# Performance work log

Hardware: AMD Instinct MI355X
Metric: run time of the kernel (lower is better)

## Reference

```python
import jax, jax.numpy as jnp
import numpy as np
import math

B, L, DIM = 2, 2048, 1024
HEADS = 16
DH = DIM // HEADS  # 64
M_IALSH = 2
U_IALSH = 0.75
NEG = -1e4  # additive mask value for non-matching hash buckets


def setup_inputs() -> dict:
    key = jax.random.key(0)
    k0, k1, k2, k3 = jax.random.split(key, 4)
    return {
        "hidden_states": jax.random.normal(k0, (B, L, DIM), jnp.float32),
        "qk_w": jax.random.normal(k1, (DIM, DIM), jnp.float32) * 0.02,
        "qk_b": jnp.zeros((DIM,), jnp.float32),
        "v_w": jax.random.normal(k2, (DIM, DIM), jnp.float32) * 0.02,
        "v_b": jnp.zeros((DIM,), jnp.float32),
        "hash_a": jax.random.normal(k3, (DH + M_IALSH,), jnp.float32),
    }


def _ialsh_mask(qkh, hash_a):
    # qkh: (b, h, l, dh). IALSH (Improved Asymmetric LSH for MIPS):
    # keys scaled so max norm per (b,h) is U; P(x)=[x, 1/2-||x||^2, 1/2-||x||^4]
    # queries unit-normalized;        Q(x)=[x/||x||, 0, 0]
    norms = jnp.linalg.norm(qkh, axis=-1, keepdims=True)          # (b,h,l,1)
    max_norm = jnp.max(norms, axis=2, keepdims=True)              # (b,h,1,1)
    xk = qkh * (U_IALSH / jnp.maximum(max_norm, 1e-12))
    nk2 = jnp.sum(xk * xk, axis=-1, keepdims=True)                # ||x||^2
    P = jnp.concatenate([xk, 0.5 - nk2, 0.5 - nk2 * nk2], axis=-1)
    q_unit = qkh / jnp.maximum(norms, 1e-12)
    zeros = jnp.zeros_like(nk2)
    Q = jnp.concatenate([q_unit, zeros, zeros], axis=-1)
    hq = (Q @ hash_a) >= 0.0                                      # (b,h,l) sign hash
    hk = (P @ hash_a) >= 0.0
    same = hq[..., :, None] == hk[..., None, :]                   # (b,h,l,l)
    return jnp.where(same, 0.0, NEG).astype(qkh.dtype)


def reference(hidden_states, qk_w, qk_b, v_w, v_b, hash_a):
    b, l, d = hidden_states.shape
    qk = hidden_states @ qk_w.T + qk_b                            # shared Q/K projection
    v = hidden_states @ v_w.T + v_b

    def split(x):  # (b,l,d) -> (b,h,l,dh)
        return x.reshape(b, l, HEADS, DH).transpose(0, 2, 1, 3)

    qkh, vh = split(qk), split(v)
    scores = jnp.einsum('bhqd,bhkd->bhqk', qkh, qkh) / math.sqrt(DH)
    scores = scores + _ialsh_mask(qkh, hash_a)
    probs = jax.nn.softmax(scores, axis=-1)  # dropout = identity (eval mode)
    ctx = jnp.einsum('bhqk,bhkd->bhqd', probs, vh)
    return ctx.transpose(0, 2, 1, 3).reshape(b, l, d)
```

## Files before the change

kernel.cpp:

```cpp
#include <hip/hip_runtime.h>

typedef unsigned short u16;
typedef unsigned char  u8;
typedef unsigned int   u32;

typedef short bf16x8 __attribute__((ext_vector_type(8)));
typedef float f32x4  __attribute__((ext_vector_type(4)));

#define DEV __device__ __forceinline__

#if __has_builtin(__builtin_amdgcn_exp2f)
#define EXP2(x) __builtin_amdgcn_exp2f(x)
#else
#define EXP2(x) exp2f(x)
#endif

DEV u16 f2bf(float x) {
  u32 u = __builtin_bit_cast(u32, x);
  u32 r = (u + 0x7fffu + ((u >> 16) & 1u)) >> 16;
  return (u16)r;
}
DEV float bf2f(u16 h) {
  u32 u = ((u32)h) << 16;
  return __builtin_bit_cast(float, u);
}
DEV f32x4 mfma16(bf16x8 a, bf16x8 b, f32x4 c) {
  return __builtin_amdgcn_mfma_f32_16x16x32_bf16(a, b, c, 0, 0, 0);
}

#define GLDS(gptr, lptr)                                                  \
  __builtin_amdgcn_global_load_lds(                                       \
      (const __attribute__((address_space(1))) void*)(gptr),              \
      (__attribute__((address_space(3))) void*)(lptr), 16, 0, 0)

__global__ __launch_bounds__(256) void split3_kernel(
    const float* __restrict__ hid, const float* __restrict__ wq,
    const float* __restrict__ wv,
    u16* __restrict__ hHi, u16* __restrict__ hLo,
    u16* __restrict__ wqHi, u16* __restrict__ wqLo, u16* __restrict__ wvHi) {
  const int NH = 4194304, NW = 1048576;
  int i = blockIdx.x * 256 + threadIdx.x;
  if (i < NH) {
    float v = hid[i];
    u16 t = f2bf(v);
    hHi[i] = t;
    hLo[i] = f2bf(v - bf2f(t));
  } else if (i < NH + NW) {
    int j = i - NH;
    float v = wq[j];
    u16 t = f2bf(v);
    wqHi[j] = t;
    wqLo[j] = f2bf(v - bf2f(t));
  } else {
    int j = i - NH - NW;
    wvHi[j] = f2bf(wv[j]);
  }
}

__global__ __launch_bounds__(256) void ca_kernel(
    const float* __restrict__ W, const float* __restrict__ ha, double* __restrict__ ca) {
  int idx = blockIdx.x * 256 + threadIdx.x;
  int h = idx >> 10, k = idx & 1023;
  double s = 0.0;
#pragma unroll 8
  for (int j = 0; j < 64; ++j)
    s += (double)W[(size_t)(h * 64 + j) * 1024 + k] * (double)ha[j];
  ca[idx] = s;
}

__global__ __launch_bounds__(256) void d_kernel(
    const float* __restrict__ hid, const double* __restrict__ ca, float* __restrict__ dq) {
  const int row  = blockIdx.x * 4 + (threadIdx.x >> 6);
  const int lane = threadIdx.x & 63;
  const int b = row >> 11, l = row & 2047;
  double acc[16];
#pragma unroll
  for (int h = 0; h < 16; ++h) acc[h] = 0.0;
  const float* hp = hid + (size_t)row * 1024;
  for (int k = lane; k < 1024; k += 64) {
    const double hv = (double)hp[k];
#pragma unroll
    for (int h = 0; h < 16; ++h) acc[h] += hv * ca[h * 1024 + k];
  }
#pragma unroll
  for (int h = 0; h < 16; ++h) {
    double v = acc[h];
#pragma unroll
    for (int off = 32; off; off >>= 1) v += __shfl_xor(v, off, 64);
    if (lane == 0) dq[(size_t)(b * 16 + h) * 2048 + l] = (float)v;
  }
}

__global__ __launch_bounds__(256, 2) void gemm_fused(
    const u16* __restrict__ hHi, const u16* __restrict__ hLo,
    const u16* __restrict__ wqHi, const u16* __restrict__ wqLo,
    const u16* __restrict__ wvHi,
    const float* __restrict__ qk_b, const float* __restrict__ v_b,
    u16* __restrict__ qkB, u16* __restrict__ vT, float* __restrict__ n2A) {
  constexpr int K = 1024;
  __shared__ u16 S[2][16384];
  const int tid = threadIdx.x, wave = tid >> 6, lane = tid & 63;
  const int quad = lane >> 4, lm = lane & 15;
  const int wr = wave >> 1, wc = wave & 1;
  const int m0 = blockIdx.x * 64, n0 = blockIdx.y * 128;
  const int ch = lane & 3, rA = lane >> 2;

  auto stage = [&](int kt, int buf) {
    const int k0 = kt * 32;
    const int rowA = wave * 16 + rA;
    GLDS(hHi + (size_t)(m0 + rowA) * K + k0 + ch * 8, &S[buf][0 + wave * 512]);
    GLDS(hLo + (size_t)(m0 + rowA) * K + k0 + ch * 8, &S[buf][2048 + wave * 512]);
#pragma unroll
    for (int it = 0; it < 2; ++it) {
      const int rb = wave * 2 + it;
      const int row = rb * 16 + rA;
      GLDS(wqHi + (size_t)(n0 + row) * K + k0 + ch * 8, &S[buf][4096 + rb * 512]);
      GLDS(wqLo + (size_t)(n0 + row) * K + k0 + ch * 8, &S[buf][8192 + rb * 512]);
      GLDS(wvHi + (size_t)(n0 + row) * K + k0 + ch * 8, &S[buf][12288 + rb * 512]);
    }
  };

  f32x4 aq[2][4], av[4][2];
#pragma unroll
  for (int i = 0; i < 2; ++i)
#pragma unroll
    for (int j = 0; j < 4; ++j) aq[i][j] = {0.f, 0.f, 0.f, 0.f};
#pragma unroll
  for (int i = 0; i < 4; ++i)
#pragma unroll
    for (int j = 0; j < 2; ++j) av[i][j] = {0.f, 0.f, 0.f, 0.f};

  stage(0, 0);
  __syncthreads();

  for (int kt = 0; kt < 32; ++kt) {
    const int cur = kt & 1;
    if (kt < 31) stage(kt + 1, cur ^ 1);

    bf16x8 a_h[2], a_l[2], b_h[4], b_l[4], w_h[4];
#pragma unroll
    for (int i = 0; i < 2; ++i) {
      a_h[i] = *(const bf16x8*)&S[cur][(wr * 32 + i * 16 + lm) * 32 + quad * 8];
      a_l[i] = *(const bf16x8*)&S[cur][2048 + (wr * 32 + i * 16 + lm) * 32 + quad * 8];
    }
#pragma unroll
    for (int j = 0; j < 4; ++j) {
      b_h[j] = *(const bf16x8*)&S[cur][4096 + (wc * 64 + j * 16 + lm) * 32 + quad * 8];
      b_l[j] = *(const bf16x8*)&S[cur][8192 + (wc * 64 + j * 16 + lm) * 32 + quad * 8];
      w_h[j] = *(const bf16x8*)&S[cur][12288 + (wc * 64 + j * 16 + lm) * 32 + quad * 8];
    }
#pragma unroll
    for (int i = 0; i < 2; ++i)
#pragma unroll
      for (int j = 0; j < 4; ++j) {
        aq[i][j] = mfma16(a_h[i], b_h[j], aq[i][j]);
        aq[i][j] = mfma16(a_h[i], b_l[j], aq[i][j]);
        aq[i][j] = mfma16(a_l[i], b_h[j], aq[i][j]);
      }
#pragma unroll
    for (int iv = 0; iv < 4; ++iv)
#pragma unroll
      for (int jv = 0; jv < 2; ++jv)
        av[iv][jv] = mfma16(w_h[iv], a_h[jv], av[iv][jv]);

    __syncthreads();
  }

  const int hidx = blockIdx.y * 2 + wc;
#pragma unroll
  for (int i = 0; i < 2; ++i) {
    float nn[4] = {0.f, 0.f, 0.f, 0.f};
#pragma unroll
    for (int j = 0; j < 4; ++j) {
      const int col = n0 + wc * 64 + j * 16 + lm;
      const float bv = qk_b[col];
#pragma unroll
      for (int r = 0; r < 4; ++r) {
        const int row = m0 + wr * 32 + i * 16 + quad * 4 + r;
        const float val = aq[i][j][r] + bv;
        qkB[(size_t)row * 1024 + col] = f2bf(val);
        nn[r] += val * val;
      }
    }
#pragma unroll
    for (int r = 0; r < 4; ++r)
#pragma unroll
      for (int off = 1; off < 16; off <<= 1) nn[r] += __shfl_xor(nn[r], off, 64);
    if (lm == 0) {
      const int row = m0 + wr * 32 + i * 16 + quad * 4;
      const int b = row >> 11, l = row & 2047;
      *(float4*)&n2A[(size_t)(b * 16 + hidx) * 2048 + l] =
          make_float4(nn[0], nn[1], nn[2], nn[3]);
    }
  }
#pragma unroll
  for (int iv = 0; iv < 4; ++iv)
#pragma unroll
    for (int r = 0; r < 4; ++r) {
      const int vcol = n0 + wc * 64 + iv * 16 + quad * 4 + r;
      const float bv = v_b[vcol];
#pragma unroll
      for (int jv = 0; jv < 2; ++jv) {
        const int tok = m0 + wr * 32 + jv * 16 + lm;
        vT[(size_t)vcol * 4096 + tok] = f2bf(av[iv][jv][r] + bv);
      }
    }
}

__global__ __launch_bounds__(256) void bits_kernel(
    const float* __restrict__ n2A, const float* __restrict__ dq,
    const float* __restrict__ ha, u8* __restrict__ hqA, u8* __restrict__ hkA) {
  const int bh = blockIdx.x;
  const int tid = threadIdx.x;
  const int wave = tid >> 6, lane = tid & 63;
  __shared__ float red[4];
  const float* n2p = n2A + (size_t)bh * 2048;
  float4 v0 = ((const float4*)n2p)[tid];
  float4 v1 = ((const float4*)n2p)[tid + 256];
  float lmax = fmaxf(fmaxf(fmaxf(v0.x, v0.y), fmaxf(v0.z, v0.w)),
                     fmaxf(fmaxf(v1.x, v1.y), fmaxf(v1.z, v1.w)));
#pragma unroll
  for (int off = 1; off < 64; off <<= 1) lmax = fmaxf(lmax, __shfl_xor(lmax, off, 64));
  if (lane == 0) red[wave] = lmax;
  __syncthreads();
  const float maxn2 = fmaxf(fmaxf(red[0], red[1]), fmaxf(red[2], red[3]));
  const float s = 0.75f / fmaxf(sqrtf(maxn2), 1e-12f);
  const float a64 = ha[64], a65 = ha[65];
#pragma unroll
  for (int it = 0; it < 8; ++it) {
    const int l = it * 256 + tid;
    const float dv = dq[(size_t)bh * 2048 + l];
    const float n2 = n2p[l];
    const float nk2 = s * s * n2;
    const float hkdot = s * dv + (0.5f - nk2) * a64 + (0.5f - nk2 * nk2) * a65;
    hqA[(size_t)bh * 2048 + l] = (dv >= 0.f) ? 1 : 0;
    hkA[(size_t)bh * 2048 + l] = (hkdot >= 0.f) ? 1 : 0;
  }
}

__global__ __launch_bounds__(256, 4) void attn_kernel(
    const u16* __restrict__ qkb, const u16* __restrict__ vT,
    const u8* __restrict__ hqA, const u8* __restrict__ hkA, float* __restrict__ out) {
  __shared__ u16 Ks[2][4096];
  __shared__ u16 Vs[2][4096];
  __shared__ u16 Ps[4][1024];

  const int qt = blockIdx.x;
  const int bh = blockIdx.y;
  const int b = bh >> 4, h = bh & 15;
  const int tid = threadIdx.x, wave = tid >> 6, lane = tid & 63;
  const int quad = lane >> 4, lm = lane & 15;
  const int lx = lm & 7;
  const int r8 = lane >> 3, ch = lane & 7;
  const int q0 = qt * 64;

  const u16* qbase = qkb + (size_t)b * 2048 * 1024 + h * 64;
  const u16* vtb = vT + (size_t)h * 64 * 4096 + b * 2048;
  const u8* hkp = hkA + (size_t)bh * 2048;

  bf16x8 aQ[2];
#pragma unroll
  for (int c = 0; c < 2; ++c)
    aQ[c] = *(const bf16x8*)(qbase +
        (size_t)(q0 + wave * 16 + lm) * 1024 + c * 32 + quad * 8);
  u8 hqb[4];
  {
    const u8* hqp = hqA + (size_t)bh * 2048 + q0 + wave * 16;
#pragma unroll
    for (int r = 0; r < 4; ++r) hqb[r] = hqp[quad * 4 + r];
  }

  const int srow = wave * 16;
  auto stage = [&](int kt, int buf) {
#pragma unroll
    for (int i = 0; i < 2; ++i) {
      const int row = srow + i * 8 + r8;
      const int sw = (ch ^ (row & 7)) * 8;
      GLDS(qbase + (size_t)(kt * 64 + row) * 1024 + sw, &Ks[buf][(srow + i * 8) * 64]);
      GLDS(vtb + (size_t)row * 4096 + kt * 64 + sw, &Vs[buf][(srow + i * 8) * 64]);
    }
  };

  stage(0, 0);

  f32x4 acc_o[4], accL;
  accL = {0.f, 0.f, 0.f, 0.f};
#pragma unroll
  for (int j = 0; j < 4; ++j) acc_o[j] = {0.f, 0.f, 0.f, 0.f};
  const bf16x8 ones = {0x3F80, 0x3F80, 0x3F80, 0x3F80, 0x3F80, 0x3F80, 0x3F80, 0x3F80};
  const float SCL = 0.18033688f;
  const float M0 = -4.3280854f;
  const float M1 = -1.4430768e4f;

  __syncthreads();

  for (int kt = 0; kt < 32; ++kt) {
    const int cur = kt & 1;
    if (kt < 31) stage(kt + 1, cur ^ 1);

    u8 hkv[4];
#pragma unroll
    for (int nb = 0; nb < 4; ++nb) hkv[nb] = hkp[kt * 64 + nb * 16 + lm];

    f32x4 cs[4];
#pragma unroll
    for (int nb = 0; nb < 4; ++nb) cs[nb] = {0.f, 0.f, 0.f, 0.f};
#pragma unroll
    for (int c = 0; c < 2; ++c)
#pragma unroll
      for (int nb = 0; nb < 4; ++nb) {
        bf16x8 bK = *(const bf16x8*)&Ks[cur][(nb * 16 + lm) * 64 + (((c * 4 + quad) ^ lx) * 8)];
        cs[nb] = mfma16(aQ[c], bK, cs[nb]);
      }

#pragma unroll
    for (int nb = 0; nb < 4; ++nb)
#pragma unroll
      for (int r = 0; r < 4; ++r) {
        const float msel = (hqb[r] == hkv[nb]) ? M0 : M1;
        const float p = EXP2(__builtin_fmaf(cs[nb][r], SCL, msel));
        const int prow = quad * 4 + r;
        const int pc = (nb * 2 + (lm >> 3)) ^ (prow & 7);
        union { float f; u16 hw[2]; } u;
        u.f = p;
        Ps[wave][prow * 64 + pc * 8 + lx] = u.hw[1];
      }

    bf16x8 aP[2];
#pragma unroll
    for (int c = 0; c < 2; ++c) {
      aP[c] = *(const bf16x8*)&Ps[wave][lm * 64 + (((c * 4 + quad) ^ lx) * 8)];
      accL = mfma16(aP[c], ones, accL);
    }
#pragma unroll
    for (int c = 0; c < 2; ++c)
#pragma unroll
      for (int j = 0; j < 4; ++j) {
        bf16x8 bV = *(const bf16x8*)&Vs[cur][(j * 16 + lm) * 64 + (((c * 4 + quad) ^ lx) * 8)];
        acc_o[j] = mfma16(aP[c], bV, acc_o[j]);
      }

    __syncthreads();
  }

#pragma unroll
  for (int r = 0; r < 4; ++r) {
    const float inv = 1.0f / accL[r];
    float* op = out + (size_t)(b * 2048 + q0 + wave * 16 + quad * 4 + r) * 1024 + h * 64;
#pragma unroll
    for (int j = 0; j < 4; ++j) op[j * 16 + lm] = acc_o[j][r] * inv;
  }
}

extern "C" void kernel_launch(void* const* d_in, const int* in_sizes, int n_in,
                              void* d_out, int out_size, void* d_ws, size_t ws_size,
                              hipStream_t stream) {
  const float* hidden = (const float*)d_in[0];
  const float* qk_w   = (const float*)d_in[1];
  const float* qk_b   = (const float*)d_in[2];
  const float* v_w    = (const float*)d_in[3];
  const float* v_b    = (const float*)d_in[4];
  const float* hash_a = (const float*)d_in[5];
  float* out = (float*)d_out;

  char* base = (char*)d_ws;
  size_t off = 0;
  auto take = [&](size_t bytes) -> char* {
    char* r = base + off;
    off += (bytes + 255) & ~(size_t)255;
    return r;
  };
  const size_t NH = 4194304;
  const size_t NW = 1048576;
  u16* hHi  = (u16*)take(NH * 2);
  u16* hLo  = (u16*)take(NH * 2);
  u16* wqHi = (u16*)take(NW * 2);
  u16* wqLo = (u16*)take(NW * 2);
  u16* wvHi = (u16*)take(NW * 2);
  u16* qkB  = (u16*)take(NH * 2);
  u16* vT   = (u16*)take(NH * 2);
  double* ca = (double*)take(16 * 1024 * 8);
  float* dq  = (float*)take(65536 * 4);
  float* n2A = (float*)take(65536 * 4);
  u8* hqA = (u8*)take(65536);
  u8* hkA = (u8*)take(65536);

  hipLaunchKernelGGL(split3_kernel, dim3((NH + 2 * NW) / 256), dim3(256), 0, stream,
                     hidden, qk_w, v_w, hHi, hLo, wqHi, wqLo, wvHi);
  hipLaunchKernelGGL(ca_kernel, dim3(64), dim3(256), 0, stream, qk_w, hash_a, ca);
  hipLaunchKernelGGL(d_kernel, dim3(1024), dim3(256), 0, stream, hidden, ca, dq);
  hipLaunchKernelGGL(gemm_fused, dim3(64, 8), dim3(256), 0, stream,
                     hHi, hLo, wqHi, wqLo, wvHi, qk_b, v_b, qkB, vT, n2A);
  hipLaunchKernelGGL(bits_kernel, dim3(32), dim3(256), 0, stream, n2A, dq, hash_a, hqA, hkA);
  hipLaunchKernelGGL(attn_kernel, dim3(32, 32), dim3(256), 0, stream, qkB, vT, hqA, hkA, out);
}
```

Before: 229.9 us.

## Switch attention kernel to 32x32x16 MFMA with 128-query tiles per block

Rewrites the attention inner loop to use 32x32x16 bf16 MFMA instructions, with each wave handling 32 query rows so a block covers 128 queries. Each loaded K/V tile is reused across twice as many queries, halving global K/V traffic per query and cutting the number of MFMA issues. The cost is more registers, doubled P scratch in LDS, a lower occupancy hint (2 blocks per CU) and half as many blocks in the grid (512 instead of 1024).

```diff
diff --git a/kernel.cpp b/kernel.cpp
--- a/kernel.cpp
+++ b/kernel.cpp
@@ -6,6 +6,7 @@
 
 typedef short bf16x8 __attribute__((ext_vector_type(8)));
 typedef float f32x4  __attribute__((ext_vector_type(4)));
+typedef float f32x16 __attribute__((ext_vector_type(16)));
 
 #define DEV __device__ __forceinline__
 
@@ -26,6 +27,9 @@
 }
 DEV f32x4 mfma16(bf16x8 a, bf16x8 b, f32x4 c) {
   return __builtin_amdgcn_mfma_f32_16x16x32_bf16(a, b, c, 0, 0, 0);
+}
+DEV f32x16 mfma32(bf16x8 a, bf16x8 b, f32x16 c) {
+  return __builtin_amdgcn_mfma_f32_32x32x16_bf16(a, b, c, 0, 0, 0);
 }
 
 #define GLDS(gptr, lptr)                                                  \
@@ -238,36 +242,36 @@
   }
 }
 
-__global__ __launch_bounds__(256, 4) void attn_kernel(
+__global__ __launch_bounds__(256, 2) void attn_kernel(
     const u16* __restrict__ qkb, const u16* __restrict__ vT,
     const u8* __restrict__ hqA, const u8* __restrict__ hkA, float* __restrict__ out) {
   __shared__ u16 Ks[2][4096];
   __shared__ u16 Vs[2][4096];
-  __shared__ u16 Ps[4][1024];
+  __shared__ u16 Ps[4][2048];
 
   const int qt = blockIdx.x;
   const int bh = blockIdx.y;
   const int b = bh >> 4, h = bh & 15;
   const int tid = threadIdx.x, wave = tid >> 6, lane = tid & 63;
-  const int quad = lane >> 4, lm = lane & 15;
-  const int lx = lm & 7;
+  const int l32 = lane & 31, half = lane >> 5;
   const int r8 = lane >> 3, ch = lane & 7;
-  const int q0 = qt * 64;
+  const int q0 = qt * 128;
 
   const u16* qbase = qkb + (size_t)b * 2048 * 1024 + h * 64;
   const u16* vtb = vT + (size_t)h * 64 * 4096 + b * 2048;
   const u8* hkp = hkA + (size_t)bh * 2048;
 
-  bf16x8 aQ[2];
-#pragma unroll
-  for (int c = 0; c < 2; ++c)
-    aQ[c] = *(const bf16x8*)(qbase +
-        (size_t)(q0 + wave * 16 + lm) * 1024 + c * 32 + quad * 8);
-  u8 hqb[4];
+  bf16x8 aQ[4];
+#pragma unroll
+  for (int kt = 0; kt < 4; ++kt)
+    aQ[kt] = *(const bf16x8*)(qbase +
+        (size_t)(q0 + wave * 32 + l32) * 1024 + kt * 16 + half * 8);
+  u8 hqb[16];
   {
-    const u8* hqp = hqA + (size_t)bh * 2048 + q0 + wave * 16;
-#pragma unroll
-    for (int r = 0; r < 4; ++r) hqb[r] = hqp[quad * 4 + r];
+    const u8* hqp = hqA + (size_t)bh * 2048 + q0 + wave * 32;
+#pragma unroll
+    for (int reg = 0; reg < 16; ++reg)
+      hqb[reg] = hqp[(reg & 3) + 8 * (reg >> 2) + 4 * half];
   }
 
   const int srow = wave * 16;
@@ -283,10 +287,9 @@
 
   stage(0, 0);
 
-  f32x4 acc_o[4], accL;
-  accL = {0.f, 0.f, 0.f, 0.f};
-#pragma unroll
-  for (int j = 0; j < 4; ++j) acc_o[j] = {0.f, 0.f, 0.f, 0.f};
+  f32x16 acc_o[2], accL;
+#pragma unroll
+  for (int e = 0; e < 16; ++e) { acc_o[0][e] = 0.f; acc_o[1][e] = 0.f; accL[e] = 0.f; }
   const bf16x8 ones = {0x3F80, 0x3F80, 0x3F80, 0x3F80, 0x3F80, 0x3F80, 0x3F80, 0x3F80};
   const float SCL = 0.18033688f;
   const float M0 = -4.3280854f;
@@ -294,61 +297,66 @@
 
   __syncthreads();
 
-  for (int kt = 0; kt < 32; ++kt) {
-    const int cur = kt & 1;
-    if (kt < 31) stage(kt + 1, cur ^ 1);
-
-    u8 hkv[4];
-#pragma unroll
-    for (int nb = 0; nb < 4; ++nb) hkv[nb] = hkp[kt * 64 + nb * 16 + lm];
-
-    f32x4 cs[4];
-#pragma unroll
-    for (int nb = 0; nb < 4; ++nb) cs[nb] = {0.f, 0.f, 0.f, 0.f};
-#pragma unroll
-    for (int c = 0; c < 2; ++c)
-#pragma unroll
-      for (int nb = 0; nb < 4; ++nb) {
-        bf16x8 bK = *(const bf16x8*)&Ks[cur][(nb * 16 + lm) * 64 + (((c * 4 + quad) ^ lx) * 8)];
-        cs[nb] = mfma16(aQ[c], bK, cs[nb]);
-      }
-
-#pragma unroll
-    for (int nb = 0; nb < 4; ++nb)
-#pragma unroll
-      for (int r = 0; r < 4; ++r) {
-        const float msel = (hqb[r] == hkv[nb]) ? M0 : M1;
-        const float p = EXP2(__builtin_fmaf(cs[nb][r], SCL, msel));
-        const int prow = quad * 4 + r;
-        const int pc = (nb * 2 + (lm >> 3)) ^ (prow & 7);
+  for (int ktile = 0; ktile < 32; ++ktile) {
+    const int cur = ktile & 1;
+    if (ktile < 31) stage(ktile + 1, cur ^ 1);
+
+    u8 hkv[2];
+#pragma unroll
+    for (int nb = 0; nb < 2; ++nb) hkv[nb] = hkp[ktile * 64 + nb * 32 + l32];
+
+    f32x16 cs[2];
+#pragma unroll
+    for (int e = 0; e < 16; ++e) { cs[0][e] = 0.f; cs[1][e] = 0.f; }
+#pragma unroll
+    for (int kt = 0; kt < 4; ++kt)
+#pragma unroll
+      for (int nb = 0; nb < 2; ++nb) {
+        const int key = nb * 32 + l32;
+        bf16x8 bK = *(const bf16x8*)&Ks[cur][key * 64 + (((kt * 2 + half) ^ (key & 7)) * 8)];
+        cs[nb] = mfma32(aQ[kt], bK, cs[nb]);
+      }
+
+#pragma unroll
+    for (int nb = 0; nb < 2; ++nb)
+#pragma unroll
+      for (int reg = 0; reg < 16; ++reg) {
+        const float msel = (hqb[reg] == hkv[nb]) ? M0 : M1;
+        const float p = EXP2(__builtin_fmaf(cs[nb][reg], SCL, msel));
+        const int prow = (reg & 3) + 8 * (reg >> 2) + 4 * half;
+        const int key = nb * 32 + l32;
+        const int pos = (key >> 3) ^ (prow & 7);
         union { float f; u16 hw[2]; } u;
         u.f = p;
-        Ps[wave][prow * 64 + pc * 8 + lx] = u.hw[1];
-      }
-
-    bf16x8 aP[2];
-#pragma unroll
-    for (int c = 0; c < 2; ++c) {
-      aP[c] = *(const bf16x8*)&Ps[wave][lm * 64 + (((c * 4 + quad) ^ lx) * 8)];
-      accL = mfma16(aP[c], ones, accL);
-    }
-#pragma unroll
-    for (int c = 0; c < 2; ++c)
-#pragma unroll
-      for (int j = 0; j < 4; ++j) {
-        bf16x8 bV = *(const bf16x8*)&Vs[cur][(j * 16 + lm) * 64 + (((c * 4 + quad) ^ lx) * 8)];
-        acc_o[j] = mfma16(aP[c], bV, acc_o[j]);
+        Ps[wave][prow * 64 + pos * 8 + (key & 7)] = u.hw[1];
+      }
+
+    bf16x8 aP[4];
+#pragma unroll
+    for (int kt = 0; kt < 4; ++kt) {
+      aP[kt] = *(const bf16x8*)&Ps[wave][l32 * 64 + (((kt * 2 + half) ^ (l32 & 7)) * 8)];
+      accL = mfma32(aP[kt], ones, accL);
+    }
+#pragma unroll
+    for (int kt = 0; kt < 4; ++kt)
+#pragma unroll
+      for (int nblk = 0; nblk < 2; ++nblk) {
+        const int d = nblk * 32 + l32;
+        bf16x8 bV = *(const bf16x8*)&Vs[cur][d * 64 + (((kt * 2 + half) ^ (d & 7)) * 8)];
+        acc_o[nblk] = mfma32(aP[kt], bV, acc_o[nblk]);
       }
 
     __syncthreads();
   }
 
 #pragma unroll
-  for (int r = 0; r < 4; ++r) {
-    const float inv = 1.0f / accL[r];
-    float* op = out + (size_t)(b * 2048 + q0 + wave * 16 + quad * 4 + r) * 1024 + h * 64;
-#pragma unroll
-    for (int j = 0; j < 4; ++j) op[j * 16 + lm] = acc_o[j][r] * inv;
+  for (int reg = 0; reg < 16; ++reg) {
+    const float inv = 1.0f / accL[reg];
+    const int qrow = q0 + wave * 32 + (reg & 3) + 8 * (reg >> 2) + 4 * half;
+    float* op = out + (size_t)(b * 2048 + qrow) * 1024 + h * 64;
+#pragma unroll
+    for (int nblk = 0; nblk < 2; ++nblk)
+      op[nblk * 32 + l32] = acc_o[nblk][reg] * inv;
   }
 }
 
@@ -392,5 +400,5 @@
   hipLaunchKernelGGL(gemm_fused, dim3(64, 8), dim3(256), 0, stream,
                      hHi, hLo, wqHi, wqLo, wvHi, qk_b, v_b, qkB, vT, n2A);
   hipLaunchKernelGGL(bits_kernel, dim3(32), dim3(256), 0, stream, n2A, dq, hash_a, hqA, hkA);
-  hipLaunchKernelGGL(attn_kernel, dim3(32, 32), dim3(256), 0, stream, qkB, vT, hqA, hkA, out);
-}
+  hipLaunchKernelGGL(attn_kernel, dim3(16, 32), dim3(256), 0, stream, qkB, vT, hqA, hkA, out);
+}
```

Result: slower. 242.4 us (+5.4%).
